# Kernel tuning notes

Measured on AMD Instinct MI355X. Metric: run time of the kernel, lower is better.

## Reference

```python
import jax, jax.numpy as jnp
import numpy as np

B, CIN, COUT, K, H, W = 8, 256, 256, 3, 64, 64
STRIDE, PAD, DIL, DG = 1, 1, 1, 1
K2 = K * K


def _conv2d(x, w, b):
    out = jax.lax.conv_general_dilated(
        x, w, (STRIDE, STRIDE), [(PAD, PAD), (PAD, PAD)],
        rhs_dilation=(DIL, DIL),
        dimension_numbers=('NCHW', 'OIHW', 'NCHW'))
    return out + b[None, :, None, None]


def _deform_conv2d(x, offset, mask, weight, bias):
    # torchvision.ops.deform_conv2d semantics (DCNv2, bilinear, zero outside).
    Bn, Cin, Hin, Win = x.shape
    O = weight.shape[0]
    dg, Cg = DG, Cin // DG
    Ho, Wo = offset.shape[2], offset.shape[3]
    # offset channel layout: [dg, K2, (dy,dx)] interleaved per kernel point
    off = offset.reshape(Bn, dg, K2, 2, Ho, Wo)
    dy, dx = off[:, :, :, 0], off[:, :, :, 1]
    m = mask.reshape(Bn, dg, K2, Ho, Wo)
    ky, kx = jnp.meshgrid(jnp.arange(K), jnp.arange(K), indexing='ij')
    ky = ky.reshape(K2).astype(x.dtype)
    kx = kx.reshape(K2).astype(x.dtype)
    base_y = jnp.arange(Ho, dtype=x.dtype) * STRIDE - PAD
    base_x = jnp.arange(Wo, dtype=x.dtype) * STRIDE - PAD
    # sampling positions [B, dg, K2, Ho, Wo]
    py = base_y[None, None, None, :, None] + (ky * DIL)[None, None, :, None, None] + dy
    px = base_x[None, None, None, None, :] + (kx * DIL)[None, None, :, None, None] + dx
    y0 = jnp.floor(py)
    x0 = jnp.floor(px)
    ly, lx = py - y0, px - x0

    xflat = x.reshape(Bn, dg, Cg, Hin * Win)

    def gather_one(xg, idx):
        return jnp.take(xg, idx, axis=1)

    gather = jax.vmap(jax.vmap(gather_one))  # over B, dg

    def corner(yc, xc, wgt):
        valid = (yc >= 0) & (yc <= Hin - 1) & (xc >= 0) & (xc <= Win - 1)
        yi = jnp.clip(yc, 0, Hin - 1).astype(jnp.int32)
        xi = jnp.clip(xc, 0, Win - 1).astype(jnp.int32)
        idx = (yi * Win + xi).reshape(Bn, dg, K2 * Ho * Wo)
        v = gather(xflat, idx).reshape(Bn, dg, Cg, K2, Ho, Wo)
        w = jnp.where(valid, wgt, jnp.zeros_like(wgt))
        return v * w[:, :, None]  # broadcast over Cg

    sampled = (corner(y0, x0, (1 - ly) * (1 - lx))
               + corner(y0, x0 + 1, (1 - ly) * lx)
               + corner(y0 + 1, x0, ly * (1 - lx))
               + corner(y0 + 1, x0 + 1, ly * lx))
    sampled = sampled * m[:, :, None]  # modulation mask
    wk = weight.reshape(O, dg, Cg, K2)
    out = jnp.einsum('ogck,bgckhw->bohw', wk, sampled)
    return out + bias[None, :, None, None]


def reference(x, weight, bias, w_off, b_off):
    om = _conv2d(x, w_off, b_off)  # [B, 3*dg*K2, H, W]
    n = DG * K2
    o1, o2, mask = om[:, :n], om[:, n:2 * n], om[:, 2 * n:]
    offset = jnp.concatenate([o1, o2], axis=1)
    mask = jax.nn.sigmoid(mask)
    return _deform_conv2d(x, offset, mask, weight, bias)


def setup_inputs():
    key = jax.random.key(0)
    k1, k2, k3, k4, k5 = jax.random.split(key, 5)
    fan_in = CIN * K2
    bound = 1.0 / np.sqrt(fan_in).astype(np.float32)
    x = jax.random.normal(k1, (B, CIN, H, W), dtype=jnp.float32)
    weight = jax.random.uniform(k2, (COUT, CIN, K, K), minval=-bound, maxval=bound, dtype=jnp.float32)
    bias = jax.random.uniform(k3, (COUT,), minval=-bound, maxval=bound, dtype=jnp.float32)
    # small random offset-conv params (zero init in the source is degenerate)
    w_off = jax.random.normal(k4, (3 * K2 * DG, CIN, K, K), dtype=jnp.float32) * 0.01
    b_off = jax.random.normal(k5, (3 * K2 * DG,), dtype=jnp.float32) * 0.01
    return {"x": x, "weight": weight, "bias": bias, "w_off": w_off, "b_off": b_off}
```

## Files before the change

### kernel.cpp

```cpp
#include <hip/hip_runtime.h>
#include <hip/hip_bf16.h>
#include <stdint.h>

typedef short bf16x8 __attribute__((ext_vector_type(8)));
typedef float f32x4  __attribute__((ext_vector_type(4)));
typedef int   i32x4  __attribute__((ext_vector_type(4)));

#define NB   8
#define NC   256
#define NO   256
#define HH   64
#define WW   64
#define NPIX 4096
#define KTOT 2304
#define NKC  72

#define XN_OFF  0u
#define XN_SZ   (NB*NPIX*NC*2u)
#define WP_OFF  (XN_OFF + XN_SZ)
#define WP_SZ   (KTOT*NO*2u)
#define WPO_OFF (WP_OFF + WP_SZ)
#define WPO_SZ  (KTOT*32u*2u)
#define OM_OFF  (WPO_OFF + WPO_SZ)
#define OM_SZ   (NB*NPIX*32u*4u)
#define PY_OFF  (OM_OFF + OM_SZ)
#define CO_SZ   (NB*9u*NPIX*4u)
#define PX_OFF  (PY_OFF + CO_SZ)
#define MK_OFF  (PX_OFF + CO_SZ)

__device__ __forceinline__ float b2f(short s) {
    union { unsigned u; float f; } z; z.u = ((unsigned)(unsigned short)s) << 16; return z.f;
}
__device__ __forceinline__ short f2b(float f) {
    __hip_bfloat16 h = __float2bfloat16(f);
    short s; __builtin_memcpy(&s, &h, 2); return s;
}
__device__ __forceinline__ float dw_lo(int u) {
    union { int i; float f; } z; z.i = u << 16; return z.f;
}
__device__ __forceinline__ float dw_hi(int u) {
    union { int i; float f; } z; z.i = u & 0xFFFF0000; return z.f;
}

__device__ __forceinline__ bf16x8 blend4(bf16x8 c0, bf16x8 c1, bf16x8 c2, bf16x8 c3,
                                         float w0, float w1, float w2, float w3) {
    union U { bf16x8 s; i32x4 i; } u0, u1, u2, u3, r;
    u0.s = c0; u1.s = c1; u2.s = c2; u3.s = c3;
#pragma unroll
    for (int d = 0; d < 4; ++d) {
        float lo = w0*dw_lo(u0.i[d]) + w1*dw_lo(u1.i[d]) + w2*dw_lo(u2.i[d]) + w3*dw_lo(u3.i[d]);
        float hi = w0*dw_hi(u0.i[d]) + w1*dw_hi(u1.i[d]) + w2*dw_hi(u2.i[d]) + w3*dw_hi(u3.i[d]);
        int pk;
        asm("v_cvt_pk_bf16_f32 %0, %1, %2" : "=v"(pk) : "v"(lo), "v"(hi));
        r.i[d] = pk;
    }
    return r.s;
}

__global__ void pack_x(const float* __restrict__ x, unsigned short* __restrict__ xn) {
    __shared__ float tile[64][65];
    int blk = blockIdx.x;
    int pt = blk & 63, ct = (blk >> 6) & 3, b = blk >> 8;
    int t = threadIdx.x;
    int ci = t >> 4, p4 = (t & 15) * 4;
    const float* src = x + ((size_t)(b*NC + ct*64))*NPIX + (size_t)pt*64;
#pragma unroll
    for (int j = 0; j < 4; ++j) {
        f32x4 v = *(const f32x4*)(src + (size_t)(ci + 16*j)*NPIX + p4);
        tile[ci + 16*j][p4+0] = v[0];
        tile[ci + 16*j][p4+1] = v[1];
        tile[ci + 16*j][p4+2] = v[2];
        tile[ci + 16*j][p4+3] = v[3];
    }
    __syncthreads();
    int c8 = (t & 7) * 8, pj0 = t >> 3;
    unsigned short* dst = xn + ((size_t)b*NPIX + (size_t)pt*64)*NC + ct*64 + c8;
#pragma unroll
    for (int j = 0; j < 2; ++j) {
        int pj = pj0 + 32*j;
        bf16x8 o;
#pragma unroll
        for (int e = 0; e < 8; ++e) o[e] = f2b(tile[c8 + e][pj]);
        *(bf16x8*)(dst + (size_t)pj*NC) = o;
    }
}

__global__ void pack_w(const float* __restrict__ weight, unsigned short* __restrict__ wp) {
    int idx = blockIdx.x*256 + threadIdx.x;
    int e = idx & 7, l = (idx >> 3) & 63, nt = (idx >> 9) & 15, kc = idx >> 13;
    int k  = kc*32 + 8*(l >> 4) + e;
    int k2 = k >> 8, c = k & 255;
    int ky = k2 / 3, kx = k2 - 3*ky;
    int o  = nt*16 + (l & 15);
    float v = weight[(size_t)(o*NC + c)*9 + ky*3 + kx];
    wp[idx] = (unsigned short)f2b(v);
}

__global__ void pack_wo(const float* __restrict__ w_off, unsigned short* __restrict__ wpo) {
    int idx = blockIdx.x*256 + threadIdx.x;
    int e = idx & 7, l = (idx >> 3) & 63, nt = (idx >> 9) & 1, kc = idx >> 10;
    int k  = kc*32 + 8*(l >> 4) + e;
    int k2 = k >> 8, c = k & 255;
    int ky = k2 / 3, kx = k2 - 3*ky;
    int n  = nt*16 + (l & 15);
    float v = (n < 27) ? w_off[(size_t)(n*NC + c)*9 + ky*3 + kx] : 0.0f;
    wpo[idx] = (unsigned short)f2b(v);
}

__launch_bounds__(256, 4)
__global__ void off_conv(const unsigned short* __restrict__ xn,
                         const unsigned short* __restrict__ wpo,
                         float* __restrict__ om) {
    int bid = blockIdx.x;
    int b = bid & 7, mt = bid >> 3;
    int t = threadIdx.x, wv = t >> 6, l = t & 63, g = l >> 4;
    int pix = mt*64 + wv*16 + (l & 15);
    int y = pix >> 6, xx = pix & 63;
    f32x4 acc0 = {0.f,0.f,0.f,0.f}, acc1 = {0.f,0.f,0.f,0.f};
    const char* xc = (const char*)(xn + (size_t)b*NPIX*NC);
    const bf16x8* wpf = (const bf16x8*)wpo;
    const bf16x8 zero8 = {0,0,0,0,0,0,0,0};
#pragma unroll
    for (int kc = 0; kc < NKC; ++kc) {
        int k2 = kc >> 3, cc = kc & 7;
        int ky = k2 / 3, kx = k2 - 3*ky;
        int sy = y + ky - 1, sx = xx + kx - 1;
        bool valid = (sy>=0)&(sy<HH)&(sx>=0)&(sx<WW);
        int cs = min(max(sy,0),HH-1)*WW + min(max(sx,0),WW-1);
        bf16x8 a = *(const bf16x8*)(xc + ((size_t)cs*NC + cc*32 + g*8)*2);
        bf16x8 w0 = wpf[(size_t)(kc*2  )*64 + l];
        bf16x8 w1 = wpf[(size_t)(kc*2+1)*64 + l];
        bf16x8 au = valid ? a : zero8;
        acc0 = __builtin_amdgcn_mfma_f32_16x16x32_bf16(au, w0, acc0, 0, 0, 0);
        acc1 = __builtin_amdgcn_mfma_f32_16x16x32_bf16(au, w1, acc1, 0, 0, 0);
    }
#pragma unroll
    for (int r = 0; r < 4; ++r) {
        int pm = mt*64 + wv*16 + 4*g + r;
        om[((size_t)b*NPIX + pm)*32 +      (l & 15)] = acc0[r];
        om[((size_t)b*NPIX + pm)*32 + 16 + (l & 15)] = acc1[r];
    }
}

__global__ void coords_k(const float* __restrict__ om, const float* __restrict__ b_off,
                         float* __restrict__ py, float* __restrict__ px,
                         float* __restrict__ mk) {
    int idx = blockIdx.x*256 + threadIdx.x;
    if (idx >= NB*9*NPIX) return;
    int pix = idx & 4095;
    int k   = (idx >> 12) % 9;
    int b   = idx / (9*NPIX);
    const float* omp = om + ((size_t)b*NPIX + pix)*32;
    float dy = omp[2*k]     + b_off[2*k];
    float dx = omp[2*k + 1] + b_off[2*k + 1];
    float m  = omp[18 + k]  + b_off[18 + k];
    float yy = (float)(pix >> 6) - 1.0f + (float)(k / 3) + dy;
    float xv = (float)(pix & 63) - 1.0f + (float)(k % 3) + dx;
    py[idx] = yy;
    px[idx] = xv;
    mk[idx] = 1.0f / (1.0f + __expf(-m));
}

__launch_bounds__(256, 2)
__global__ void dcn_main(const unsigned short* __restrict__ xn,
                         const unsigned short* __restrict__ wpack,
                         const float* __restrict__ pyA,
                         const float* __restrict__ pxA,
                         const float* __restrict__ mkA,
                         const float* __restrict__ bias,
                         float* __restrict__ out) {
    __shared__ char lds[2][32768];
    int bid = blockIdx.x;
    int b  = bid & 7;
    int u  = bid >> 3;
    int nh = u & 1, mt = u >> 1;
    int t = threadIdx.x, wv = t >> 6, l = t & 63, g = l >> 4;
    int pix0 = mt*128 + wv*32 + (l & 15);

    f32x4 acc[2][8];
#pragma unroll
    for (int f = 0; f < 2; ++f)
#pragma unroll
        for (int nt = 0; nt < 8; ++nt) acc[f][nt] = f32x4{0.f,0.f,0.f,0.f};

    const char* xc = (const char*)(xn + (size_t)b*NPIX*NC);

    auto coord_compute = [&](float py, float px, float m, float* cwf, const char** bpf) {
        float y0f = floorf(py), x0f = floorf(px);
        float ly = py - y0f, lx = px - x0f;
        int iy0 = (int)y0f, ix0 = (int)x0f;
        int iy1 = iy0 + 1,  ix1 = ix0 + 1;
        bool vy0 = (iy0 >= 0) & (iy0 < HH);
        bool vy1 = (iy1 >= 0) & (iy1 < HH);
        bool vx0 = (ix0 >= 0) & (ix0 < WW);
        bool vx1 = (ix1 >= 0) & (ix1 < WW);
        float wy0 = (1.f - ly) * m, wy1 = ly * m;
        cwf[0] = (vy0 & vx0) ? wy0 * (1.f - lx) : 0.f;
        cwf[1] = (vy0 & vx1) ? wy0 * lx         : 0.f;
        cwf[2] = (vy1 & vx0) ? wy1 * (1.f - lx) : 0.f;
        cwf[3] = (vy1 & vx1) ? wy1 * lx         : 0.f;
        int cy0 = min(max(iy0,0),HH-1), cy1 = min(max(iy1,0),HH-1);
        int cx0 = min(max(ix0,0),WW-1), cx1 = min(max(ix1,0),WW-1);
        bpf[0] = xc + ((size_t)(cy0*WW + cx0)*NC + g*8)*2;
        bpf[1] = xc + ((size_t)(cy0*WW + cx1)*NC + g*8)*2;
        bpf[2] = xc + ((size_t)(cy1*WW + cx0)*NC + g*8)*2;
        bpf[3] = xc + ((size_t)(cy1*WW + cx1)*NC + g*8)*2;
    };

    auto stage = [&](int buf, int ph) {
        int k2 = ph >> 1, h = ph & 1;
        int kcp = k2*8 + h*4 + wv;
        const unsigned short* gs = wpack + ((size_t)(kcp*16 + nh*8))*512 + l*8;
        char* ld = &lds[buf][wv*8192];
#pragma unroll
        for (int i = 0; i < 8; ++i) {
            __builtin_amdgcn_global_load_lds(
                (const __attribute__((address_space(1))) unsigned int*)(gs + i*512),
                (__attribute__((address_space(3))) unsigned int*)(ld + i*1024),
                16, 0, 0);
        }
    };

    stage(0, 0);
    __syncthreads();

    for (int ph = 0; ph < 18; ++ph) {
        int buf = ph & 1;
        if (ph < 17) stage(buf ^ 1, ph + 1);
        int k2 = ph >> 1, h = ph & 1;

        float cw[2][4]; const char* bp[2][4];
#pragma unroll
        for (int f = 0; f < 2; ++f) {
            int ci = ((b*9 + k2) << 12) + pix0 + f*16;
            coord_compute(pyA[ci], pxA[ci], mkA[ci], cw[f], bp[f]);
        }
#pragma unroll
        for (int s = 0; s < 4; ++s) {
            int cb = (h*4 + s)*64;
            bf16x8 af[2];
#pragma unroll
            for (int f = 0; f < 2; ++f) {
                bf16x8 c0 = *(const bf16x8*)(bp[f][0] + cb);
                bf16x8 c1 = *(const bf16x8*)(bp[f][1] + cb);
                bf16x8 c2 = *(const bf16x8*)(bp[f][2] + cb);
                bf16x8 c3 = *(const bf16x8*)(bp[f][3] + cb);
                af[f] = blend4(c0, c1, c2, c3, cw[f][0], cw[f][1], cw[f][2], cw[f][3]);
            }
            const char* blp = &lds[buf][s*8192];
#pragma unroll
            for (int nt = 0; nt < 8; ++nt) {
                bf16x8 wf = *(const bf16x8*)(blp + nt*1024 + l*16);
                acc[0][nt] = __builtin_amdgcn_mfma_f32_16x16x32_bf16(af[0], wf, acc[0][nt], 0, 0, 0);
                acc[1][nt] = __builtin_amdgcn_mfma_f32_16x16x32_bf16(af[1], wf, acc[1][nt], 0, 0, 0);
            }
        }
        __syncthreads();
    }

    int pmbase = mt*128 + wv*32 + 4*g;
#pragma unroll
    for (int f = 0; f < 2; ++f)
#pragma unroll
        for (int nt = 0; nt < 8; ++nt) {
            int o = nh*128 + nt*16 + (l & 15);
            float bv = bias[o];
            f32x4 r = acc[f][nt] + bv;
            *(f32x4*)(out + ((size_t)(b*NO + o))*NPIX + pmbase + f*16) = r;
        }
}

extern "C" void kernel_launch(void* const* d_in, const int* in_sizes, int n_in,
                              void* d_out, int out_size, void* d_ws, size_t ws_size,
                              hipStream_t stream) {
    const float* x      = (const float*)d_in[0];
    const float* weight = (const float*)d_in[1];
    const float* bias   = (const float*)d_in[2];
    const float* w_off  = (const float*)d_in[3];
    const float* b_off  = (const float*)d_in[4];
    float* out = (float*)d_out;
    char* ws = (char*)d_ws;

    unsigned short* xn  = (unsigned short*)(ws + XN_OFF);
    unsigned short* wp  = (unsigned short*)(ws + WP_OFF);
    unsigned short* wpo = (unsigned short*)(ws + WPO_OFF);
    float* om = (float*)(ws + OM_OFF);
    float* py = (float*)(ws + PY_OFF);
    float* px = (float*)(ws + PX_OFF);
    float* mk = (float*)(ws + MK_OFF);

    pack_x  <<<2048, 256, 0, stream>>>(x, xn);
    pack_w  <<<KTOT*NO/256,  256, 0, stream>>>(weight, wp);
    pack_wo <<<KTOT*32/256,  256, 0, stream>>>(w_off, wpo);
    off_conv<<<512, 256, 0, stream>>>(xn, wpo, om);
    coords_k<<<NB*9*NPIX/256, 256, 0, stream>>>(om, b_off, py, px, mk);
    dcn_main<<<512, 256, 0, stream>>>(xn, wp, py, px, mk, bias, out);
}
```

Baseline: 264.0 us.

## Split K across waves in DCN GEMM with LDS reduction; split offset-conv N across waves

The main deformable-conv kernel now gives each of the four waves a quarter of the K dimension (18 of 72 chunks) for a 32-pixel by 128-channel tile. It reads weights straight from global memory instead of staging them in LDS, then reduces the partial sums through LDS in a two-step tree. The grid grows from 512 to 2048 blocks and the launch bound rises to 3 blocks per SM, for more parallelism and fewer per-step barriers. The offset conv splits its two N halves across waves, doubling the grid. The cost is more redundant bilinear gathers per output, uncached weight loads, and reduction traffic through LDS.

```diff
diff --git a/kernel.cpp b/kernel.cpp
--- a/kernel.cpp
+++ b/kernel.cpp
@@ -112,11 +112,13 @@
                          const unsigned short* __restrict__ wpo,
                          float* __restrict__ om) {
     int bid = blockIdx.x;
-    int b = bid & 7, mt = bid >> 3;
-    int t = threadIdx.x, wv = t >> 6, l = t & 63, g = l >> 4;
-    int pix = mt*64 + wv*16 + (l & 15);
+    int b = bid & 7, rr = bid >> 3;
+    int t = threadIdx.x, wv = t >> 6, l = t & 63, g = l >> 4, l15 = l & 15;
+    int wid = rr*4 + wv;
+    int mt = wid >> 1, nh = wid & 1;
+    int pix = mt*16 + l15;
     int y = pix >> 6, xx = pix & 63;
-    f32x4 acc0 = {0.f,0.f,0.f,0.f}, acc1 = {0.f,0.f,0.f,0.f};
+    f32x4 acc = {0.f,0.f,0.f,0.f};
     const char* xc = (const char*)(xn + (size_t)b*NPIX*NC);
     const bf16x8* wpf = (const bf16x8*)wpo;
     const bf16x8 zero8 = {0,0,0,0,0,0,0,0};
@@ -128,17 +130,13 @@
         bool valid = (sy>=0)&(sy<HH)&(sx>=0)&(sx<WW);
         int cs = min(max(sy,0),HH-1)*WW + min(max(sx,0),WW-1);
         bf16x8 a = *(const bf16x8*)(xc + ((size_t)cs*NC + cc*32 + g*8)*2);
-        bf16x8 w0 = wpf[(size_t)(kc*2  )*64 + l];
-        bf16x8 w1 = wpf[(size_t)(kc*2+1)*64 + l];
-        bf16x8 au = valid ? a : zero8;
-        acc0 = __builtin_amdgcn_mfma_f32_16x16x32_bf16(au, w0, acc0, 0, 0, 0);
-        acc1 = __builtin_amdgcn_mfma_f32_16x16x32_bf16(au, w1, acc1, 0, 0, 0);
+        bf16x8 w = wpf[(size_t)(kc*2 + nh)*64 + l];
+        acc = __builtin_amdgcn_mfma_f32_16x16x32_bf16(valid ? a : zero8, w, acc, 0, 0, 0);
     }
 #pragma unroll
     for (int r = 0; r < 4; ++r) {
-        int pm = mt*64 + wv*16 + 4*g + r;
-        om[((size_t)b*NPIX + pm)*32 +      (l & 15)] = acc0[r];
-        om[((size_t)b*NPIX + pm)*32 + 16 + (l & 15)] = acc1[r];
+        int pm = mt*16 + 4*g + r;
+        om[((size_t)b*NPIX + pm)*32 + nh*16 + l15] = acc[r];
     }
 }
 
@@ -161,7 +159,8 @@
     mk[idx] = 1.0f / (1.0f + __expf(-m));
 }
 
-__launch_bounds__(256, 2)
+#define RST 132
+__launch_bounds__(256, 3)
 __global__ void dcn_main(const unsigned short* __restrict__ xn,
                          const unsigned short* __restrict__ wpack,
                          const float* __restrict__ pyA,
@@ -169,13 +168,14 @@
                          const float* __restrict__ mkA,
                          const float* __restrict__ bias,
                          float* __restrict__ out) {
-    __shared__ char lds[2][32768];
+    __shared__ float red[2][32*RST];
     int bid = blockIdx.x;
     int b  = bid & 7;
     int u  = bid >> 3;
     int nh = u & 1, mt = u >> 1;
-    int t = threadIdx.x, wv = t >> 6, l = t & 63, g = l >> 4;
-    int pix0 = mt*128 + wv*32 + (l & 15);
+    int t = threadIdx.x, l = t & 63, g = l >> 4, l15 = l & 15;
+    int wv = __builtin_amdgcn_readfirstlane(t >> 6);
+    int pix0 = mt*32 + l15;
 
     f32x4 acc[2][8];
 #pragma unroll
@@ -185,89 +185,113 @@
 
     const char* xc = (const char*)(xn + (size_t)b*NPIX*NC);
 
-    auto coord_compute = [&](float py, float px, float m, float* cwf, const char** bpf) {
-        float y0f = floorf(py), x0f = floorf(px);
-        float ly = py - y0f, lx = px - x0f;
-        int iy0 = (int)y0f, ix0 = (int)x0f;
-        int iy1 = iy0 + 1,  ix1 = ix0 + 1;
-        bool vy0 = (iy0 >= 0) & (iy0 < HH);
-        bool vy1 = (iy1 >= 0) & (iy1 < HH);
-        bool vx0 = (ix0 >= 0) & (ix0 < WW);
-        bool vx1 = (ix1 >= 0) & (ix1 < WW);
-        float wy0 = (1.f - ly) * m, wy1 = ly * m;
-        cwf[0] = (vy0 & vx0) ? wy0 * (1.f - lx) : 0.f;
-        cwf[1] = (vy0 & vx1) ? wy0 * lx         : 0.f;
-        cwf[2] = (vy1 & vx0) ? wy1 * (1.f - lx) : 0.f;
-        cwf[3] = (vy1 & vx1) ? wy1 * lx         : 0.f;
-        int cy0 = min(max(iy0,0),HH-1), cy1 = min(max(iy1,0),HH-1);
-        int cx0 = min(max(ix0,0),WW-1), cx1 = min(max(ix1,0),WW-1);
-        bpf[0] = xc + ((size_t)(cy0*WW + cx0)*NC + g*8)*2;
-        bpf[1] = xc + ((size_t)(cy0*WW + cx1)*NC + g*8)*2;
-        bpf[2] = xc + ((size_t)(cy1*WW + cx0)*NC + g*8)*2;
-        bpf[3] = xc + ((size_t)(cy1*WW + cx1)*NC + g*8)*2;
-    };
-
-    auto stage = [&](int buf, int ph) {
-        int k2 = ph >> 1, h = ph & 1;
-        int kcp = k2*8 + h*4 + wv;
-        const unsigned short* gs = wpack + ((size_t)(kcp*16 + nh*8))*512 + l*8;
-        char* ld = &lds[buf][wv*8192];
-#pragma unroll
-        for (int i = 0; i < 8; ++i) {
-            __builtin_amdgcn_global_load_lds(
-                (const __attribute__((address_space(1))) unsigned int*)(gs + i*512),
-                (__attribute__((address_space(3))) unsigned int*)(ld + i*1024),
-                16, 0, 0);
+    float cw[2][4];
+    unsigned co[2][4];
+
+    auto coord_compute = [&](int k2) {
+#pragma unroll
+        for (int f = 0; f < 2; ++f) {
+            int ci = ((b*9 + k2) << 12) + pix0 + f*16;
+            float py = pyA[ci], px = pxA[ci], m = mkA[ci];
+            float y0f = floorf(py), x0f = floorf(px);
+            float ly = py - y0f, lx = px - x0f;
+            int iy0 = (int)y0f, ix0 = (int)x0f;
+            int iy1 = iy0 + 1,  ix1 = ix0 + 1;
+            bool vy0 = (iy0 >= 0) & (iy0 < HH);
+            bool vy1 = (iy1 >= 0) & (iy1 < HH);
+            bool vx0 = (ix0 >= 0) & (ix0 < WW);
+            bool vx1 = (ix1 >= 0) & (ix1 < WW);
+            float wy0 = (1.f - ly) * m, wy1 = ly * m;
+            cw[f][0] = (vy0 & vx0) ? wy0 * (1.f - lx) : 0.f;
+            cw[f][1] = (vy0 & vx1) ? wy0 * lx         : 0.f;
+            cw[f][2] = (vy1 & vx0) ? wy1 * (1.f - lx) : 0.f;
+            cw[f][3] = (vy1 & vx1) ? wy1 * lx         : 0.f;
+            int cy0 = min(max(iy0,0),HH-1), cy1 = min(max(iy1,0),HH-1);
+            int cx0 = min(max(ix0,0),WW-1), cx1 = min(max(ix1,0),WW-1);
+            co[f][0] = (unsigned)(((cy0*WW + cx0)*NC + g*8) * 2);
+            co[f][1] = (unsigned)(((cy0*WW + cx1)*NC + g*8) * 2);
+            co[f][2] = (unsigned)(((cy1*WW + cx0)*NC + g*8) * 2);
+            co[f][3] = (unsigned)(((cy1*WW + cx1)*NC + g*8) * 2);
         }
     };
 
-    stage(0, 0);
-    __syncthreads();
-
-    for (int ph = 0; ph < 18; ++ph) {
-        int buf = ph & 1;
-        if (ph < 17) stage(buf ^ 1, ph + 1);
-        int k2 = ph >> 1, h = ph & 1;
-
-        float cw[2][4]; const char* bp[2][4];
+    {
+        int kcg0 = wv*18;
+        coord_compute(kcg0 >> 3);
+    }
+#pragma unroll
+    for (int tt = 0; tt < 18; ++tt) {
+        int kcg = wv*18 + tt;
+        int k2 = kcg >> 3, cc = kcg & 7;
+        if (tt > 0 && cc == 0) coord_compute(k2);
+        unsigned cb = (unsigned)cc * 64u;
+        const bf16x8* wf = (const bf16x8*)wpack + ((size_t)kcg*16 + nh*8)*64 + l;
+        bf16x8 af[2];
 #pragma unroll
         for (int f = 0; f < 2; ++f) {
-            int ci = ((b*9 + k2) << 12) + pix0 + f*16;
-            coord_compute(pyA[ci], pxA[ci], mkA[ci], cw[f], bp[f]);
+            bf16x8 c0 = *(const bf16x8*)(xc + co[f][0] + cb);
+            bf16x8 c1 = *(const bf16x8*)(xc + co[f][1] + cb);
+            bf16x8 c2 = *(const bf16x8*)(xc + co[f][2] + cb);
+            bf16x8 c3 = *(const bf16x8*)(xc + co[f][3] + cb);
+            af[f] = blend4(c0, c1, c2, c3, cw[f][0], cw[f][1], cw[f][2], cw[f][3]);
         }
 #pragma unroll
-        for (int s = 0; s < 4; ++s) {
-            int cb = (h*4 + s)*64;
-            bf16x8 af[2];
-#pragma unroll
-            for (int f = 0; f < 2; ++f) {
-                bf16x8 c0 = *(const bf16x8*)(bp[f][0] + cb);
-                bf16x8 c1 = *(const bf16x8*)(bp[f][1] + cb);
-                bf16x8 c2 = *(const bf16x8*)(bp[f][2] + cb);
-                bf16x8 c3 = *(const bf16x8*)(bp[f][3] + cb);
-                af[f] = blend4(c0, c1, c2, c3, cw[f][0], cw[f][1], cw[f][2], cw[f][3]);
+        for (int nt = 0; nt < 8; ++nt) {
+            bf16x8 w = wf[nt*64];
+            acc[0][nt] = __builtin_amdgcn_mfma_f32_16x16x32_bf16(af[0], w, acc[0][nt], 0, 0, 0);
+            acc[1][nt] = __builtin_amdgcn_mfma_f32_16x16x32_bf16(af[1], w, acc[1][nt], 0, 0, 0);
+        }
+    }
+
+    __syncthreads();
+    if (wv >= 2) {
+        float* s = red[wv - 2];
+#pragma unroll
+        for (int f = 0; f < 2; ++f)
+#pragma unroll
+            for (int nt = 0; nt < 8; ++nt)
+#pragma unroll
+                for (int r = 0; r < 4; ++r)
+                    s[(f*16 + 4*g + r)*RST + nt*16 + l15] = acc[f][nt][r];
+    }
+    __syncthreads();
+    if (wv < 2) {
+        const float* s = red[wv];
+#pragma unroll
+        for (int f = 0; f < 2; ++f)
+#pragma unroll
+            for (int nt = 0; nt < 8; ++nt)
+#pragma unroll
+                for (int r = 0; r < 4; ++r)
+                    acc[f][nt][r] += s[(f*16 + 4*g + r)*RST + nt*16 + l15];
+    }
+    __syncthreads();
+    if (wv == 1) {
+        float* s = red[0];
+#pragma unroll
+        for (int f = 0; f < 2; ++f)
+#pragma unroll
+            for (int nt = 0; nt < 8; ++nt)
+#pragma unroll
+                for (int r = 0; r < 4; ++r)
+                    s[(f*16 + 4*g + r)*RST + nt*16 + l15] = acc[f][nt][r];
+    }
+    __syncthreads();
+    if (wv == 0) {
+        const float* s = red[0];
+#pragma unroll
+        for (int f = 0; f < 2; ++f)
+#pragma unroll
+            for (int nt = 0; nt < 8; ++nt) {
+                int o = nh*128 + nt*16 + l15;
+                float bv = bias[o];
+                f32x4 r = acc[f][nt];
+#pragma unroll
+                for (int rr = 0; rr < 4; ++rr)
+                    r[rr] += s[(f*16 + 4*g + rr)*RST + nt*16 + l15] + bv;
+                *(f32x4*)(out + ((size_t)(b*NO + o))*NPIX + mt*32 + f*16 + 4*g) = r;
             }
-            const char* blp = &lds[buf][s*8192];
-#pragma unroll
-            for (int nt = 0; nt < 8; ++nt) {
-                bf16x8 wf = *(const bf16x8*)(blp + nt*1024 + l*16);
-                acc[0][nt] = __builtin_amdgcn_mfma_f32_16x16x32_bf16(af[0], wf, acc[0][nt], 0, 0, 0);
-                acc[1][nt] = __builtin_amdgcn_mfma_f32_16x16x32_bf16(af[1], wf, acc[1][nt], 0, 0, 0);
-            }
-        }
-        __syncthreads();
-    }
-
-    int pmbase = mt*128 + wv*32 + 4*g;
-#pragma unroll
-    for (int f = 0; f < 2; ++f)
-#pragma unroll
-        for (int nt = 0; nt < 8; ++nt) {
-            int o = nh*128 + nt*16 + (l & 15);
-            float bv = bias[o];
-            f32x4 r = acc[f][nt] + bv;
-            *(f32x4*)(out + ((size_t)(b*NO + o))*NPIX + pmbase + f*16) = r;
-        }
+    }
 }
 
 extern "C" void kernel_launch(void* const* d_in, const int* in_sizes, int n_in,
@@ -292,7 +316,7 @@
     pack_x  <<<2048, 256, 0, stream>>>(x, xn);
     pack_w  <<<KTOT*NO/256,  256, 0, stream>>>(weight, wp);
     pack_wo <<<KTOT*32/256,  256, 0, stream>>>(w_off, wpo);
-    off_conv<<<512, 256, 0, stream>>>(xn, wpo, om);
+    off_conv<<<1024, 256, 0, stream>>>(xn, wpo, om);
     coords_k<<<NB*9*NPIX/256, 256, 0, stream>>>(om, b_off, py, px, mk);
-    dcn_main<<<512, 256, 0, stream>>>(xn, wp, py, px, mk, bias, out);
-}
+    dcn_main<<<2048, 256, 0, stream>>>(xn, wp, py, px, mk, bias, out);
+}
```

Result: slower. 317.5 us (+20.3%).
